# Kernel optimization log

Measured on AMD Instinct MI355X. Metric: run time of the kernel, lower is better.

The kernel has to match this reference:

```python
import jax, jax.numpy as jnp
import numpy as np

N_NODES = 50000
N_EDGES = 1_600_000
IN_CH = 128
HIDDEN = 64
OUT_CH = 1


def glorot(key, shape):
    limit = np.sqrt(6.0 / (shape[0] + shape[1]))
    return jax.random.uniform(key, shape, jnp.float32, -limit, limit)


def setup_inputs() -> dict:
    key = jax.random.key(0)
    ks = jax.random.split(key, 6)
    x = jax.random.normal(ks[0], (N_NODES, IN_CH), jnp.float32)
    edge_index = jax.random.randint(ks[1], (2, N_EDGES), 0, N_NODES, jnp.int64)
    W1 = glorot(ks[2], (IN_CH, HIDDEN))
    b1 = jnp.zeros((HIDDEN,), jnp.float32)
    W2 = glorot(ks[3], (HIDDEN, HIDDEN // 2))
    b2 = jnp.zeros((HIDDEN // 2,), jnp.float32)
    Wh = glorot(ks[4], (HIDDEN // 2, OUT_CH))
    bh = jnp.zeros((OUT_CH,), jnp.float32)
    return {"x": x, "edge_index": edge_index, "W1": W1, "b1": b1,
            "W2": W2, "b2": b2, "Wh": Wh, "bh": bh}


def gcn_conv(x, src, dst, W, b):
    """PyG-style GCNConv: H' = D^{-1/2} (A + I) D^{-1/2} X W + b."""
    n = x.shape[0]
    h = x @ W  # transform first (smaller message dim)
    # degree of A + I (all edge weights = 1, self-loop weight = 1)
    deg = jax.ops.segment_sum(jnp.ones(src.shape[0], h.dtype), dst,
                              num_segments=n) + 1.0
    dinv = deg ** -0.5
    norm = dinv[src] * dinv[dst]                      # [E]
    msg = h[src] * norm[:, None]                      # [E, F] gather
    agg = jax.ops.segment_sum(msg, dst, num_segments=n)  # scatter-add
    agg = agg + h * (dinv * dinv)[:, None]            # self-loop term
    return agg + b


def reference(x, edge_index, W1, b1, W2, b2, Wh, bh):
    src, dst = edge_index[0], edge_index[1]
    h = jax.nn.relu(gcn_conv(x, src, dst, W1, b1))
    # dropout: inference mode (training=False) -> identity
    h = jax.nn.relu(gcn_conv(h, src, dst, W2, b2))
    return h @ Wh + bh
```

## Files before the change

kernel.cpp:

```cpp
#include <hip/hip_runtime.h>

#define N_NODES 50000
#define IN_CH 128
#define HID 64
#define HID2 32

constexpr int NB = 391;
constexpr int CHUNK = 4096;
constexpr int CAP = 5120;
#define FPSCALE 524288.0f
#define FPINV   0x1p-19f

__device__ __forceinline__ unsigned short f2bf(float f) {
    union { float f; unsigned u; } v; v.f = f;
    unsigned r = v.u + 0x7fff + ((v.u >> 16) & 1);
    return (unsigned short)(r >> 16);
}
__device__ __forceinline__ float bflo(unsigned d) {
    union { unsigned u; float f; } v; v.u = d << 16; return v.f;
}
__device__ __forceinline__ float bfhi(unsigned d) {
    union { unsigned u; float f; } v; v.u = d & 0xffff0000u; return v.f;
}

__global__ __launch_bounds__(256) void bin_kernel(const int* __restrict__ src,
                                                  const int* __restrict__ dst,
                                                  int* __restrict__ bcur,
                                                  unsigned short* __restrict__ psrc,
                                                  unsigned char* __restrict__ pbyte, int E) {
    __shared__ int hist[NB], lbase[NB], gbase[NB], lcur[NB];
    __shared__ unsigned short outs[CHUNK];
    __shared__ int outd[CHUNK];
    int tid = threadIdx.x;
    int base = blockIdx.x * CHUNK;
    int cnt = min(CHUNK, E - base);
    for (int i = tid; i < NB; i += 256) hist[i] = 0;
    int es[CHUNK / 256], ed[CHUNK / 256];
    __syncthreads();
#pragma unroll
    for (int k = 0; k < CHUNK / 256; k++) {
        int e = base + k * 256 + tid;
        if (e < E) {
            es[k] = src[e];
            ed[k] = dst[e];
            atomicAdd(&hist[ed[k] >> 7], 1);
        }
    }
    __syncthreads();
    if (tid == 0) {
        int run = 0;
        for (int b = 0; b < NB; b++) { int t = hist[b]; lbase[b] = run; run += t; }
    }
    __syncthreads();
    for (int i = tid; i < NB; i += 256) {
        gbase[i] = i * CAP + (hist[i] ? atomicAdd(&bcur[i], hist[i]) : 0);
        lcur[i] = lbase[i];
    }
    __syncthreads();
#pragma unroll
    for (int k = 0; k < CHUNK / 256; k++) {
        int e = base + k * 256 + tid;
        if (e < E) {
            int b = ed[k] >> 7;
            int p = atomicAdd(&lcur[b], 1);
            outs[p] = (unsigned short)es[k];
            outd[p] = ed[k];
        }
    }
    __syncthreads();
#pragma unroll
    for (int k = 0; k < CHUNK / 256; k++) {
        int i = k * 256 + tid;
        if (i < cnt) {
            int d = outd[i];
            int b = d >> 7;
            int gp = gbase[b] + (i - lbase[b]);
            psrc[gp] = outs[i];
            pbyte[gp] = (unsigned char)(d & 127);
        }
    }
}

__global__ __launch_bounds__(256) void fine_kernel(unsigned short* __restrict__ psrc,
                                                   const unsigned char* __restrict__ pbyte,
                                                   const int* __restrict__ bcur,
                                                   int* __restrict__ off,
                                                   unsigned short* __restrict__ len,
                                                   float* __restrict__ dinv, int N) {
    __shared__ unsigned short lsrc[CAP];
    __shared__ unsigned char lb[CAP];
    __shared__ int fh[128], fb[128], fc[128];
    int b = blockIdx.x, tid = threadIdx.x;
    int gb = b * CAP;
    int cnt = min(bcur[b], CAP);
    if (tid < 128) fh[tid] = 0;
    __syncthreads();
    for (int i = tid; i < cnt; i += 256) {
        lsrc[i] = psrc[gb + i];
        int dl = pbyte[gb + i];
        lb[i] = (unsigned char)dl;
        atomicAdd(&fh[dl], 1);
    }
    __syncthreads();
    if (tid == 0) {
        int run = 0;
        for (int j = 0; j < 128; j++) { int t = fh[j]; fb[j] = run; run += t; }
    }
    __syncthreads();
    if (tid < 128) {
        fc[tid] = fb[tid];
        int node = (b << 7) + tid;
        if (node < N) {
            off[node] = gb + fb[tid];
            len[node] = (unsigned short)fh[tid];
            dinv[node] = rsqrtf((float)fh[tid] + 1.0f);
        }
    }
    __syncthreads();
    for (int i = tid; i < cnt; i += 256) {
        int p = atomicAdd(&fc[lb[i]], 1);
        psrc[gb + p] = lsrc[i];
    }
}

template <int K, int J, int NPB>
__global__ __launch_bounds__(256) void gemm_s_kernel(const float* __restrict__ X,
                                                     const float* __restrict__ W,
                                                     const float* __restrict__ dinv,
                                                     unsigned short* __restrict__ out, int N) {
    constexpr int QJ = J / 4;
    constexpr int NPT = NPB / (256 / QJ);
    static_assert(NPT == 2, "layout assumes 2 nodes/thread");
    constexpr int RG = K / 4;
    constexpr int RS = K + 4;
    __shared__ float Ws[K * J];
    __shared__ float Xs[NPB * RS];
    int tid = threadIdx.x;
    for (int i = tid; i < K * J / 4; i += 256) ((float4*)Ws)[i] = ((const float4*)W)[i];
    int n0 = blockIdx.x * NPB;
    for (int i = tid; i < NPB * RG; i += 256) {
        int r = i / RG, c = i % RG;
        int n = n0 + r;
        float4 v = make_float4(0.f, 0.f, 0.f, 0.f);
        if (n < N) v = ((const float4*)(X + (size_t)n * K))[c];
        *(float4*)&Xs[r * RS + ((c ^ (r & 7)) << 2)] = v;
    }
    __syncthreads();
    int q = tid % QJ, g = (tid / QJ) * NPT;
    const float* xr0 = &Xs[g * RS];
    const float* xr1 = &Xs[(g + 1) * RS];
    int sw0 = g & 7, sw1 = (g + 1) & 7;
    float4 a0 = make_float4(0.f, 0.f, 0.f, 0.f);
    float4 a1 = make_float4(0.f, 0.f, 0.f, 0.f);
#pragma unroll 8
    for (int k = 0; k < K; k++) {
        float4 w = *(const float4*)&Ws[k * J + q * 4];
        float x0 = xr0[(((k >> 2) ^ sw0) << 2) + (k & 3)];
        float x1 = xr1[(((k >> 2) ^ sw1) << 2) + (k & 3)];
        a0.x += x0 * w.x; a0.y += x0 * w.y; a0.z += x0 * w.z; a0.w += x0 * w.w;
        a1.x += x1 * w.x; a1.y += x1 * w.y; a1.z += x1 * w.z; a1.w += x1 * w.w;
    }
    int n = n0 + g;
    if (n < N) {
        float d0 = dinv[n] * FPSCALE;
        ushort4 o = make_ushort4(f2bf(a0.x * d0), f2bf(a0.y * d0),
                                 f2bf(a0.z * d0), f2bf(a0.w * d0));
        *(ushort4*)(out + (size_t)n * J + q * 4) = o;
    }
    if (n + 1 < N) {
        float d1 = dinv[n + 1] * FPSCALE;
        ushort4 o = make_ushort4(f2bf(a1.x * d1), f2bf(a1.y * d1),
                                 f2bf(a1.z * d1), f2bf(a1.w * d1));
        *(ushort4*)(out + (size_t)(n + 1) * J + q * 4) = o;
    }
}

__global__ __launch_bounds__(256) void agg1_kernel(const unsigned short* __restrict__ sorted_src,
                                                   const int* __restrict__ off,
                                                   const unsigned short* __restrict__ len,
                                                   const float* __restrict__ dinv,
                                                   const unsigned short* __restrict__ xws,
                                                   const float* __restrict__ b1,
                                                   float* __restrict__ h1, int N) {
    int lane = threadIdx.x & 63;
    int n = blockIdx.x * 4 + (threadIdx.x >> 6);
    if (n >= N) return;
    int g = lane >> 3, fl = lane & 7;
    int start = off[n], end = start + len[n];
    int acc[8] = {0, 0, 0, 0, 0, 0, 0, 0};
    int i = start + g;
    for (; i + 8 < end; i += 16) {
        int s0 = sorted_src[i], s1 = sorted_src[i + 8];
        uint4 q0 = *(const uint4*)(xws + (size_t)s0 * HID + fl * 8);
        uint4 q1 = *(const uint4*)(xws + (size_t)s1 * HID + fl * 8);
        acc[0] += (int)bflo(q0.x) + (int)bflo(q1.x);
        acc[1] += (int)bfhi(q0.x) + (int)bfhi(q1.x);
        acc[2] += (int)bflo(q0.y) + (int)bflo(q1.y);
        acc[3] += (int)bfhi(q0.y) + (int)bfhi(q1.y);
        acc[4] += (int)bflo(q0.z) + (int)bflo(q1.z);
        acc[5] += (int)bfhi(q0.z) + (int)bfhi(q1.z);
        acc[6] += (int)bflo(q0.w) + (int)bflo(q1.w);
        acc[7] += (int)bfhi(q0.w) + (int)bfhi(q1.w);
    }
    if (i < end) {
        int s = sorted_src[i];
        uint4 q = *(const uint4*)(xws + (size_t)s * HID + fl * 8);
        acc[0] += (int)bflo(q.x); acc[1] += (int)bfhi(q.x);
        acc[2] += (int)bflo(q.y); acc[3] += (int)bfhi(q.y);
        acc[4] += (int)bflo(q.z); acc[5] += (int)bfhi(q.z);
        acc[6] += (int)bflo(q.w); acc[7] += (int)bfhi(q.w);
    }
#pragma unroll
    for (int m = 8; m <= 32; m <<= 1)
#pragma unroll
        for (int j = 0; j < 8; j++) acc[j] += __shfl_xor(acc[j], m, 64);
    if (g == 0) {
        float dis = dinv[n] * FPINV;
        uint4 q = *(const uint4*)(xws + (size_t)n * HID + fl * 8);
        int sv[8] = {(int)bflo(q.x), (int)bfhi(q.x), (int)bflo(q.y), (int)bfhi(q.y),
                     (int)bflo(q.z), (int)bfhi(q.z), (int)bflo(q.w), (int)bfhi(q.w)};
        float4 bb0 = *(const float4*)(b1 + fl * 8);
        float4 bb1 = *(const float4*)(b1 + fl * 8 + 4);
        float bbv[8] = {bb0.x, bb0.y, bb0.z, bb0.w, bb1.x, bb1.y, bb1.z, bb1.w};
        float o[8];
#pragma unroll
        for (int j = 0; j < 8; j++)
            o[j] = fmaxf((float)(acc[j] + sv[j]) * dis + bbv[j], 0.f);
        *(float4*)(h1 + (size_t)n * HID + fl * 8)     = make_float4(o[0], o[1], o[2], o[3]);
        *(float4*)(h1 + (size_t)n * HID + fl * 8 + 4) = make_float4(o[4], o[5], o[6], o[7]);
    }
}

__global__ __launch_bounds__(256) void agg2_final_kernel(const unsigned short* __restrict__ sorted_src,
                                                         const int* __restrict__ off,
                                                         const unsigned short* __restrict__ len,
                                                         const float* __restrict__ dinv,
                                                         const unsigned short* __restrict__ hws,
                                                         const float* __restrict__ b2,
                                                         const float* __restrict__ Wh,
                                                         const float* __restrict__ bh,
                                                         float* __restrict__ out, int N) {
    int lane = threadIdx.x & 63;
    int n = blockIdx.x * 4 + (threadIdx.x >> 6);
    if (n >= N) return;
    int g = lane >> 2, fl = lane & 3;
    int start = off[n], end = start + len[n];
    int acc[8] = {0, 0, 0, 0, 0, 0, 0, 0};
    int i = start + g;
    for (; i + 16 < end; i += 32) {
        int s0 = sorted_src[i], s1 = sorted_src[i + 16];
        uint4 q0 = *(const uint4*)(hws + (size_t)s0 * HID2 + fl * 8);
        uint4 q1 = *(const uint4*)(hws + (size_t)s1 * HID2 + fl * 8);
        acc[0] += (int)bflo(q0.x) + (int)bflo(q1.x);
        acc[1] += (int)bfhi(q0.x) + (int)bfhi(q1.x);
        acc[2] += (int)bflo(q0.y) + (int)bflo(q1.y);
        acc[3] += (int)bfhi(q0.y) + (int)bfhi(q1.y);
        acc[4] += (int)bflo(q0.z) + (int)bflo(q1.z);
        acc[5] += (int)bfhi(q0.z) + (int)bfhi(q1.z);
        acc[6] += (int)bflo(q0.w) + (int)bflo(q1.w);
        acc[7] += (int)bfhi(q0.w) + (int)bfhi(q1.w);
    }
    if (i < end) {
        int s = sorted_src[i];
        uint4 q = *(const uint4*)(hws + (size_t)s * HID2 + fl * 8);
        acc[0] += (int)bflo(q.x); acc[1] += (int)bfhi(q.x);
        acc[2] += (int)bflo(q.y); acc[3] += (int)bfhi(q.y);
        acc[4] += (int)bflo(q.z); acc[5] += (int)bfhi(q.z);
        acc[6] += (int)bflo(q.w); acc[7] += (int)bfhi(q.w);
    }
#pragma unroll
    for (int m = 4; m <= 32; m <<= 1)
#pragma unroll
        for (int j = 0; j < 8; j++) acc[j] += __shfl_xor(acc[j], m, 64);
    float dis = dinv[n] * FPINV;
    uint4 q = *(const uint4*)(hws + (size_t)n * HID2 + fl * 8);
    int sv[8] = {(int)bflo(q.x), (int)bfhi(q.x), (int)bflo(q.y), (int)bfhi(q.y),
                 (int)bflo(q.z), (int)bfhi(q.z), (int)bflo(q.w), (int)bfhi(q.w)};
    float4 bb0 = *(const float4*)(b2 + fl * 8);
    float4 bb1 = *(const float4*)(b2 + fl * 8 + 4);
    float bbv[8] = {bb0.x, bb0.y, bb0.z, bb0.w, bb1.x, bb1.y, bb1.z, bb1.w};
    float4 wv0 = *(const float4*)(Wh + fl * 8);
    float4 wv1 = *(const float4*)(Wh + fl * 8 + 4);
    float wvv[8] = {wv0.x, wv0.y, wv0.z, wv0.w, wv1.x, wv1.y, wv1.z, wv1.w};
    float p = 0.f;
#pragma unroll
    for (int j = 0; j < 8; j++)
        p += fmaxf((float)(acc[j] + sv[j]) * dis + bbv[j], 0.f) * wvv[j];
    p += __shfl_xor(p, 1, 64);
    p += __shfl_xor(p, 2, 64);
    if (lane == 0) out[n] = p + bh[0];
}

extern "C" void kernel_launch(void* const* d_in, const int* in_sizes, int n_in,
                              void* d_out, int out_size, void* d_ws, size_t ws_size,
                              hipStream_t stream) {
    const float* x  = (const float*)d_in[0];
    const int*   ei = (const int*)d_in[1];
    const float* W1 = (const float*)d_in[2];
    const float* b1 = (const float*)d_in[3];
    const float* W2 = (const float*)d_in[4];
    const float* b2 = (const float*)d_in[5];
    const float* Wh = (const float*)d_in[6];
    const float* bh = (const float*)d_in[7];
    float* out = (float*)d_out;

    const int N = N_NODES;
    const int E = in_sizes[1] / 2;
    const int* src = ei;
    const int* dst = ei + E;

    int* ws = (int*)d_ws;
    int*            bcur  = ws;
    int*            off   = bcur + 512;
    unsigned short* len   = (unsigned short*)(off + 50048);
    float*          dinv  = (float*)((int*)len + 25024);
    unsigned short* psrc  = (unsigned short*)(dinv + 50048);
    unsigned char*  pbyte = (unsigned char*)(psrc + (size_t)NB * CAP);
    unsigned short* xws   = (unsigned short*)(pbyte + (size_t)NB * CAP);
    float*          h1    = (float*)(xws + (size_t)N * HID);
    unsigned short* hws   = xws;

    hipMemsetAsync(bcur, 0, NB * sizeof(int), stream);

    int eblocks = (E + CHUNK - 1) / CHUNK;
    bin_kernel<<<eblocks, 256, 0, stream>>>(src, dst, bcur, psrc, pbyte, E);
    fine_kernel<<<NB, 256, 0, stream>>>(psrc, pbyte, bcur, off, len, dinv, N);

    gemm_s_kernel<IN_CH, HID, 32><<<(N + 31) / 32, 256, 0, stream>>>(x, W1, dinv, xws, N);
    agg1_kernel<<<(N + 3) / 4, 256, 0, stream>>>(psrc, off, len, dinv, xws, b1, h1, N);

    gemm_s_kernel<HID, HID2, 64><<<(N + 63) / 64, 256, 0, stream>>>(h1, W2, dinv, hws, N);
    agg2_final_kernel<<<(N + 3) / 4, 256, 0, stream>>>(psrc, off, len, dinv, hws, b2, Wh, bh, out, N);
}
```

Before: 211.8 us.

## Fuse layer-1 aggregation with the W2 GEMM and pack bin-sort scratch

The layer-1 aggregation now also applies ReLU, multiplies each node's 64-wide hidden row by W2 held in shared memory, and writes the scaled bf16 hws directly. This drops the fp32 h1 round-trip through global memory and removes the separate gemm_s launch. Each wave now gathers in two 32-column passes with 16 edge groups instead of one 64-column pass with 8. Every block reloads the 8 KB W2 into shared memory and runs a serial 64-step dot product per output. Separately, the bin kernel packs src and dst into one 32-bit shared-memory word to cut LDS traffic.

```diff
diff --git a/kernel.cpp b/kernel.cpp
--- a/kernel.cpp
+++ b/kernel.cpp
@@ -29,8 +29,7 @@
                                                   unsigned short* __restrict__ psrc,
                                                   unsigned char* __restrict__ pbyte, int E) {
     __shared__ int hist[NB], lbase[NB], gbase[NB], lcur[NB];
-    __shared__ unsigned short outs[CHUNK];
-    __shared__ int outd[CHUNK];
+    __shared__ unsigned outp[CHUNK];
     int tid = threadIdx.x;
     int base = blockIdx.x * CHUNK;
     int cnt = min(CHUNK, E - base);
@@ -63,8 +62,7 @@
         if (e < E) {
             int b = ed[k] >> 7;
             int p = atomicAdd(&lcur[b], 1);
-            outs[p] = (unsigned short)es[k];
-            outd[p] = ed[k];
+            outp[p] = ((unsigned)es[k] << 16) | (unsigned)ed[k];
         }
     }
     __syncthreads();
@@ -72,10 +70,11 @@
     for (int k = 0; k < CHUNK / 256; k++) {
         int i = k * 256 + tid;
         if (i < cnt) {
-            int d = outd[i];
+            unsigned p = outp[i];
+            int d = (int)(p & 0xffffu);
             int b = d >> 7;
             int gp = gbase[b] + (i - lbase[b]);
-            psrc[gp] = outs[i];
+            psrc[gp] = (unsigned short)(p >> 16);
             pbyte[gp] = (unsigned char)(d & 127);
         }
     }
@@ -175,60 +174,79 @@
     }
 }
 
-__global__ __launch_bounds__(256) void agg1_kernel(const unsigned short* __restrict__ sorted_src,
-                                                   const int* __restrict__ off,
-                                                   const unsigned short* __restrict__ len,
-                                                   const float* __restrict__ dinv,
-                                                   const unsigned short* __restrict__ xws,
-                                                   const float* __restrict__ b1,
-                                                   float* __restrict__ h1, int N) {
-    int lane = threadIdx.x & 63;
-    int n = blockIdx.x * 4 + (threadIdx.x >> 6);
-    if (n >= N) return;
-    int g = lane >> 3, fl = lane & 7;
-    int start = off[n], end = start + len[n];
-    int acc[8] = {0, 0, 0, 0, 0, 0, 0, 0};
-    int i = start + g;
-    for (; i + 8 < end; i += 16) {
-        int s0 = sorted_src[i], s1 = sorted_src[i + 8];
-        uint4 q0 = *(const uint4*)(xws + (size_t)s0 * HID + fl * 8);
-        uint4 q1 = *(const uint4*)(xws + (size_t)s1 * HID + fl * 8);
-        acc[0] += (int)bflo(q0.x) + (int)bflo(q1.x);
-        acc[1] += (int)bfhi(q0.x) + (int)bfhi(q1.x);
-        acc[2] += (int)bflo(q0.y) + (int)bflo(q1.y);
-        acc[3] += (int)bfhi(q0.y) + (int)bfhi(q1.y);
-        acc[4] += (int)bflo(q0.z) + (int)bflo(q1.z);
-        acc[5] += (int)bfhi(q0.z) + (int)bfhi(q1.z);
-        acc[6] += (int)bflo(q0.w) + (int)bflo(q1.w);
-        acc[7] += (int)bfhi(q0.w) + (int)bfhi(q1.w);
-    }
-    if (i < end) {
-        int s = sorted_src[i];
-        uint4 q = *(const uint4*)(xws + (size_t)s * HID + fl * 8);
-        acc[0] += (int)bflo(q.x); acc[1] += (int)bfhi(q.x);
-        acc[2] += (int)bflo(q.y); acc[3] += (int)bfhi(q.y);
-        acc[4] += (int)bflo(q.z); acc[5] += (int)bfhi(q.z);
-        acc[6] += (int)bflo(q.w); acc[7] += (int)bfhi(q.w);
-    }
-#pragma unroll
-    for (int m = 8; m <= 32; m <<= 1)
-#pragma unroll
-        for (int j = 0; j < 8; j++) acc[j] += __shfl_xor(acc[j], m, 64);
-    if (g == 0) {
-        float dis = dinv[n] * FPINV;
-        uint4 q = *(const uint4*)(xws + (size_t)n * HID + fl * 8);
-        int sv[8] = {(int)bflo(q.x), (int)bfhi(q.x), (int)bflo(q.y), (int)bfhi(q.y),
-                     (int)bflo(q.z), (int)bfhi(q.z), (int)bflo(q.w), (int)bfhi(q.w)};
-        float4 bb0 = *(const float4*)(b1 + fl * 8);
-        float4 bb1 = *(const float4*)(b1 + fl * 8 + 4);
-        float bbv[8] = {bb0.x, bb0.y, bb0.z, bb0.w, bb1.x, bb1.y, bb1.z, bb1.w};
-        float o[8];
-#pragma unroll
-        for (int j = 0; j < 8; j++)
-            o[j] = fmaxf((float)(acc[j] + sv[j]) * dis + bbv[j], 0.f);
-        *(float4*)(h1 + (size_t)n * HID + fl * 8)     = make_float4(o[0], o[1], o[2], o[3]);
-        *(float4*)(h1 + (size_t)n * HID + fl * 8 + 4) = make_float4(o[4], o[5], o[6], o[7]);
-    }
+__global__ __launch_bounds__(256) void agg1_fused_kernel(const unsigned short* __restrict__ sorted_src,
+                                                         const int* __restrict__ off,
+                                                         const unsigned short* __restrict__ len,
+                                                         const float* __restrict__ dinv,
+                                                         const unsigned short* __restrict__ xws,
+                                                         const float* __restrict__ b1,
+                                                         const float* __restrict__ W2,
+                                                         unsigned short* __restrict__ hws, int N) {
+    __shared__ float W2s[HID * HID2];
+    __shared__ float hrow[4][HID];
+    int tid = threadIdx.x;
+    for (int i = tid; i < HID * HID2 / 4; i += 256)
+        ((float4*)W2s)[i] = ((const float4*)W2)[i];
+    int wid = tid >> 6, lane = tid & 63;
+    int n = blockIdx.x * 4 + wid;
+    bool valid = (n < N);
+    int nn = valid ? n : (N - 1);
+    int g = lane >> 2, fl = lane & 3;
+    int start = off[nn], end = start + len[nn];
+    float dis = dinv[nn] * FPINV;
+#pragma unroll
+    for (int h = 0; h < 2; h++) {
+        int colOff = h * 32 + fl * 8;
+        int acc[8] = {0, 0, 0, 0, 0, 0, 0, 0};
+        int i = start + g;
+        for (; i + 16 < end; i += 32) {
+            int s0 = sorted_src[i], s1 = sorted_src[i + 16];
+            uint4 q0 = *(const uint4*)(xws + (size_t)s0 * HID + colOff);
+            uint4 q1 = *(const uint4*)(xws + (size_t)s1 * HID + colOff);
+            acc[0] += (int)bflo(q0.x) + (int)bflo(q1.x);
+            acc[1] += (int)bfhi(q0.x) + (int)bfhi(q1.x);
+            acc[2] += (int)bflo(q0.y) + (int)bflo(q1.y);
+            acc[3] += (int)bfhi(q0.y) + (int)bfhi(q1.y);
+            acc[4] += (int)bflo(q0.z) + (int)bflo(q1.z);
+            acc[5] += (int)bfhi(q0.z) + (int)bfhi(q1.z);
+            acc[6] += (int)bflo(q0.w) + (int)bflo(q1.w);
+            acc[7] += (int)bfhi(q0.w) + (int)bfhi(q1.w);
+        }
+        if (i < end) {
+            int s = sorted_src[i];
+            uint4 q = *(const uint4*)(xws + (size_t)s * HID + colOff);
+            acc[0] += (int)bflo(q.x); acc[1] += (int)bfhi(q.x);
+            acc[2] += (int)bflo(q.y); acc[3] += (int)bfhi(q.y);
+            acc[4] += (int)bflo(q.z); acc[5] += (int)bfhi(q.z);
+            acc[6] += (int)bflo(q.w); acc[7] += (int)bfhi(q.w);
+        }
+#pragma unroll
+        for (int m = 4; m <= 32; m <<= 1)
+#pragma unroll
+            for (int j = 0; j < 8; j++) acc[j] += __shfl_xor(acc[j], m, 64);
+        if (g == 0) {
+            uint4 q = *(const uint4*)(xws + (size_t)nn * HID + colOff);
+            int sv[8] = {(int)bflo(q.x), (int)bfhi(q.x), (int)bflo(q.y), (int)bfhi(q.y),
+                         (int)bflo(q.z), (int)bfhi(q.z), (int)bflo(q.w), (int)bfhi(q.w)};
+            float4 bb0 = *(const float4*)(b1 + colOff);
+            float4 bb1 = *(const float4*)(b1 + colOff + 4);
+            float bbv[8] = {bb0.x, bb0.y, bb0.z, bb0.w, bb1.x, bb1.y, bb1.z, bb1.w};
+            float o[8];
+#pragma unroll
+            for (int j = 0; j < 8; j++)
+                o[j] = fmaxf((float)(acc[j] + sv[j]) * dis + bbv[j], 0.f);
+            *(float4*)&hrow[wid][colOff]     = make_float4(o[0], o[1], o[2], o[3]);
+            *(float4*)&hrow[wid][colOff + 4] = make_float4(o[4], o[5], o[6], o[7]);
+        }
+    }
+    __syncthreads();
+    int j = lane & 31;
+    float p = 0.f;
+#pragma unroll 8
+    for (int k = 0; k < HID; k++)
+        p += hrow[wid][k] * W2s[k * HID2 + j];
+    if (valid && lane < 32)
+        hws[(size_t)n * HID2 + j] = f2bf(p * dinv[n] * FPSCALE);
 }
 
 __global__ __launch_bounds__(256) void agg2_final_kernel(const unsigned short* __restrict__ sorted_src,
@@ -317,8 +335,7 @@
     unsigned short* psrc  = (unsigned short*)(dinv + 50048);
     unsigned char*  pbyte = (unsigned char*)(psrc + (size_t)NB * CAP);
     unsigned short* xws   = (unsigned short*)(pbyte + (size_t)NB * CAP);
-    float*          h1    = (float*)(xws + (size_t)N * HID);
-    unsigned short* hws   = xws;
+    unsigned short* hws   = xws + (size_t)N * HID;
 
     hipMemsetAsync(bcur, 0, NB * sizeof(int), stream);
 
@@ -327,8 +344,6 @@
     fine_kernel<<<NB, 256, 0, stream>>>(psrc, pbyte, bcur, off, len, dinv, N);
 
     gemm_s_kernel<IN_CH, HID, 32><<<(N + 31) / 32, 256, 0, stream>>>(x, W1, dinv, xws, N);
-    agg1_kernel<<<(N + 3) / 4, 256, 0, stream>>>(psrc, off, len, dinv, xws, b1, h1, N);
-
-    gemm_s_kernel<HID, HID2, 64><<<(N + 63) / 64, 256, 0, stream>>>(h1, W2, dinv, hws, N);
+    agg1_fused_kernel<<<(N + 3) / 4, 256, 0, stream>>>(psrc, off, len, dinv, xws, b1, W2, hws, N);
     agg2_final_kernel<<<(N + 3) / 4, 256, 0, stream>>>(psrc, off, len, dinv, hws, b2, Wh, bh, out, N);
 }
```

New measurement: 235.8 us. 1.11x slower.

## Fuse second-layer GEMM into first aggregation and widen binning kernels

Applied to the files above, without the earlier changes.

The first-layer aggregation now keeps each node's ReLU output in shared memory and immediately multiplies it by W2. It writes the scaled bf16 hidden features directly, so the fp32 h1 buffer and the separate second GEMM launch are gone. The binning and fine-sort kernels move from 256 to 1024 threads per block, and the bin kernel packs the src/dst pair into one 32-bit shared-memory word instead of two arrays. The fused GEMM has every lane read W2 from global memory with half the lanes doing duplicate work. It also relies on intra-wave ordering of the shared-memory row without an explicit barrier.

```diff
diff --git a/kernel.cpp b/kernel.cpp
--- a/kernel.cpp
+++ b/kernel.cpp
@@ -23,23 +23,22 @@
     union { unsigned u; float f; } v; v.u = d & 0xffff0000u; return v.f;
 }
 
-__global__ __launch_bounds__(256) void bin_kernel(const int* __restrict__ src,
-                                                  const int* __restrict__ dst,
-                                                  int* __restrict__ bcur,
-                                                  unsigned short* __restrict__ psrc,
-                                                  unsigned char* __restrict__ pbyte, int E) {
+__global__ __launch_bounds__(1024) void bin_kernel(const int* __restrict__ src,
+                                                   const int* __restrict__ dst,
+                                                   int* __restrict__ bcur,
+                                                   unsigned short* __restrict__ psrc,
+                                                   unsigned char* __restrict__ pbyte, int E) {
     __shared__ int hist[NB], lbase[NB], gbase[NB], lcur[NB];
-    __shared__ unsigned short outs[CHUNK];
-    __shared__ int outd[CHUNK];
+    __shared__ unsigned outp[CHUNK];
     int tid = threadIdx.x;
     int base = blockIdx.x * CHUNK;
     int cnt = min(CHUNK, E - base);
-    for (int i = tid; i < NB; i += 256) hist[i] = 0;
-    int es[CHUNK / 256], ed[CHUNK / 256];
-    __syncthreads();
-#pragma unroll
-    for (int k = 0; k < CHUNK / 256; k++) {
-        int e = base + k * 256 + tid;
+    for (int i = tid; i < NB; i += 1024) hist[i] = 0;
+    int es[CHUNK / 1024], ed[CHUNK / 1024];
+    __syncthreads();
+#pragma unroll
+    for (int k = 0; k < CHUNK / 1024; k++) {
+        int e = base + k * 1024 + tid;
         if (e < E) {
             es[k] = src[e];
             ed[k] = dst[e];
@@ -52,41 +51,41 @@
         for (int b = 0; b < NB; b++) { int t = hist[b]; lbase[b] = run; run += t; }
     }
     __syncthreads();
-    for (int i = tid; i < NB; i += 256) {
+    for (int i = tid; i < NB; i += 1024) {
         gbase[i] = i * CAP + (hist[i] ? atomicAdd(&bcur[i], hist[i]) : 0);
         lcur[i] = lbase[i];
     }
     __syncthreads();
 #pragma unroll
-    for (int k = 0; k < CHUNK / 256; k++) {
-        int e = base + k * 256 + tid;
+    for (int k = 0; k < CHUNK / 1024; k++) {
+        int e = base + k * 1024 + tid;
         if (e < E) {
             int b = ed[k] >> 7;
             int p = atomicAdd(&lcur[b], 1);
-            outs[p] = (unsigned short)es[k];
-            outd[p] = ed[k];
+            outp[p] = ((unsigned)es[k] << 16) | (unsigned)ed[k];
         }
     }
     __syncthreads();
 #pragma unroll
-    for (int k = 0; k < CHUNK / 256; k++) {
-        int i = k * 256 + tid;
+    for (int k = 0; k < CHUNK / 1024; k++) {
+        int i = k * 1024 + tid;
         if (i < cnt) {
-            int d = outd[i];
+            unsigned p = outp[i];
+            int d = (int)(p & 0xffffu);
             int b = d >> 7;
             int gp = gbase[b] + (i - lbase[b]);
-            psrc[gp] = outs[i];
+            psrc[gp] = (unsigned short)(p >> 16);
             pbyte[gp] = (unsigned char)(d & 127);
         }
     }
 }
 
-__global__ __launch_bounds__(256) void fine_kernel(unsigned short* __restrict__ psrc,
-                                                   const unsigned char* __restrict__ pbyte,
-                                                   const int* __restrict__ bcur,
-                                                   int* __restrict__ off,
-                                                   unsigned short* __restrict__ len,
-                                                   float* __restrict__ dinv, int N) {
+__global__ __launch_bounds__(1024) void fine_kernel(unsigned short* __restrict__ psrc,
+                                                    const unsigned char* __restrict__ pbyte,
+                                                    const int* __restrict__ bcur,
+                                                    int* __restrict__ off,
+                                                    unsigned short* __restrict__ len,
+                                                    float* __restrict__ dinv, int N) {
     __shared__ unsigned short lsrc[CAP];
     __shared__ unsigned char lb[CAP];
     __shared__ int fh[128], fb[128], fc[128];
@@ -95,7 +94,7 @@
     int cnt = min(bcur[b], CAP);
     if (tid < 128) fh[tid] = 0;
     __syncthreads();
-    for (int i = tid; i < cnt; i += 256) {
+    for (int i = tid; i < cnt; i += 1024) {
         lsrc[i] = psrc[gb + i];
         int dl = pbyte[gb + i];
         lb[i] = (unsigned char)dl;
@@ -117,7 +116,7 @@
         }
     }
     __syncthreads();
-    for (int i = tid; i < cnt; i += 256) {
+    for (int i = tid; i < cnt; i += 1024) {
         int p = atomicAdd(&fc[lb[i]], 1);
         psrc[gb + p] = lsrc[i];
     }
@@ -175,15 +174,17 @@
     }
 }
 
-__global__ __launch_bounds__(256) void agg1_kernel(const unsigned short* __restrict__ sorted_src,
-                                                   const int* __restrict__ off,
-                                                   const unsigned short* __restrict__ len,
-                                                   const float* __restrict__ dinv,
-                                                   const unsigned short* __restrict__ xws,
-                                                   const float* __restrict__ b1,
-                                                   float* __restrict__ h1, int N) {
-    int lane = threadIdx.x & 63;
-    int n = blockIdx.x * 4 + (threadIdx.x >> 6);
+__global__ __launch_bounds__(256) void agg1_fused_kernel(const unsigned short* __restrict__ sorted_src,
+                                                         const int* __restrict__ off,
+                                                         const unsigned short* __restrict__ len,
+                                                         const float* __restrict__ dinv,
+                                                         const unsigned short* __restrict__ xws,
+                                                         const float* __restrict__ b1,
+                                                         const float* __restrict__ W2,
+                                                         unsigned short* __restrict__ hws, int N) {
+    __shared__ float hrow[4][HID];
+    int tid = threadIdx.x, wid = tid >> 6, lane = tid & 63;
+    int n = blockIdx.x * 4 + wid;
     if (n >= N) return;
     int g = lane >> 3, fl = lane & 7;
     int start = off[n], end = start + len[n];
@@ -226,9 +227,16 @@
 #pragma unroll
         for (int j = 0; j < 8; j++)
             o[j] = fmaxf((float)(acc[j] + sv[j]) * dis + bbv[j], 0.f);
-        *(float4*)(h1 + (size_t)n * HID + fl * 8)     = make_float4(o[0], o[1], o[2], o[3]);
-        *(float4*)(h1 + (size_t)n * HID + fl * 8 + 4) = make_float4(o[4], o[5], o[6], o[7]);
-    }
+        *(float4*)&hrow[wid][fl * 8]     = make_float4(o[0], o[1], o[2], o[3]);
+        *(float4*)&hrow[wid][fl * 8 + 4] = make_float4(o[4], o[5], o[6], o[7]);
+    }
+    int j = lane & 31;
+    float p = 0.f;
+#pragma unroll 8
+    for (int k = 0; k < HID; k++)
+        p += hrow[wid][k] * W2[k * HID2 + j];
+    if (lane < 32)
+        hws[(size_t)n * HID2 + j] = f2bf(p * dinv[n] * FPSCALE);
 }
 
 __global__ __launch_bounds__(256) void agg2_final_kernel(const unsigned short* __restrict__ sorted_src,
@@ -317,18 +325,15 @@
     unsigned short* psrc  = (unsigned short*)(dinv + 50048);
     unsigned char*  pbyte = (unsigned char*)(psrc + (size_t)NB * CAP);
     unsigned short* xws   = (unsigned short*)(pbyte + (size_t)NB * CAP);
-    float*          h1    = (float*)(xws + (size_t)N * HID);
-    unsigned short* hws   = xws;
+    unsigned short* hws   = xws + (size_t)N * HID;
 
     hipMemsetAsync(bcur, 0, NB * sizeof(int), stream);
 
     int eblocks = (E + CHUNK - 1) / CHUNK;
-    bin_kernel<<<eblocks, 256, 0, stream>>>(src, dst, bcur, psrc, pbyte, E);
-    fine_kernel<<<NB, 256, 0, stream>>>(psrc, pbyte, bcur, off, len, dinv, N);
+    bin_kernel<<<eblocks, 1024, 0, stream>>>(src, dst, bcur, psrc, pbyte, E);
+    fine_kernel<<<NB, 1024, 0, stream>>>(psrc, pbyte, bcur, off, len, dinv, N);
 
     gemm_s_kernel<IN_CH, HID, 32><<<(N + 31) / 32, 256, 0, stream>>>(x, W1, dinv, xws, N);
-    agg1_kernel<<<(N + 3) / 4, 256, 0, stream>>>(psrc, off, len, dinv, xws, b1, h1, N);
-
-    gemm_s_kernel<HID, HID2, 64><<<(N + 63) / 64, 256, 0, stream>>>(h1, W2, dinv, hws, N);
+    agg1_fused_kernel<<<(N + 3) / 4, 256, 0, stream>>>(psrc, off, len, dinv, xws, b1, W2, hws, N);
     agg2_final_kernel<<<(N + 3) / 4, 256, 0, stream>>>(psrc, off, len, dinv, hws, b2, Wh, bh, out, N);
 }
```

New measurement: 213.1 us. About the same (+0.6%).
